# Optimization experiments

Hardware: AMD Instinct MI355X
Metric: run time of the kernel (lower is better)

The kernel has to match this reference:

```python
import jax, jax.numpy as jnp
import numpy as np

M = 0.4
S = 64.0
EPS = 1e-5

def _normalize(x, axis=-1):
    n = jnp.linalg.norm(x, axis=axis, keepdims=True)
    return x / jnp.maximum(n, EPS)

def setup_inputs() -> dict:
    key = jax.random.key(0)
    k1, k2, k3 = jax.random.split(key, 3)
    B, D, C = 512, 512, 100000
    inp = jax.random.normal(k1, (B, D), dtype=jnp.float32)
    weight = jax.random.normal(k2, (C, D), dtype=jnp.float32) * (D ** -0.5)
    label = jax.random.randint(k3, (B,), 0, C, dtype=jnp.int64)
    bias = jnp.full((1,), float(np.log(C * 10)), dtype=jnp.float32)
    return {"input": inp, "label": label, "weight": weight, "bias": bias}

def reference(input, label, weight, bias):
    # cos_theta: [B, C]
    cos_theta = _normalize(input) @ _normalize(weight).T
    cos_m_theta_p = S * (cos_theta - M) - bias
    cos_m_theta_n = S * cos_theta - bias
    # log(1 + exp(x)) with clamp to [-S, S] as in the original
    p_loss = jnp.log1p(jnp.exp(-jnp.clip(cos_m_theta_p, -S, S)))
    n_loss = jnp.log1p(jnp.exp(jnp.clip(cos_m_theta_n, -S, S)))
    one_hot = jax.nn.one_hot(label, cos_theta.shape[1], dtype=jnp.bool_)
    losses = jnp.where(one_hot, p_loss, n_loss)
    return losses.sum(axis=1).mean()
```

## Files before the change

### kernel.cpp

```cpp
#include <hip/hip_runtime.h>
#include <hip/hip_bf16.h>
#include <stdint.h>

#define C_CLS  100000
#define DDIM   512
#define BROWS  512
#define NT     64
#define NSTEP  16
#define EPSN   1e-5f

typedef __attribute__((ext_vector_type(8))) short short8;
typedef __attribute__((ext_vector_type(4))) float f32x4;


__device__ inline unsigned pk2(float a, float b) {
  __hip_bfloat162 h = __float22bfloat162_rn(make_float2(a, b));
  unsigned u; __builtin_memcpy(&u, &h, 4); return u;
}

__global__ void __launch_bounds__(64) k_norm_input(const float* __restrict__ in,
                                                   uint4* __restrict__ xnf,
                                                   float* __restrict__ ws) {
  int b = blockIdx.x;
  int lane = threadIdx.x;
  if (lane == 0) {
    if (b < 256) ws[b * 16] = 0.f;
    else if (b < 320) ws[4096 + (b - 256) * 16] = 0.f;
  }
  const float4* row = (const float4*)(in + b * DDIM);
  float4 v0 = row[lane * 2];
  float4 v1 = row[lane * 2 + 1];
  float ss = v0.x*v0.x + v0.y*v0.y + v0.z*v0.z + v0.w*v0.w
           + v1.x*v1.x + v1.y*v1.y + v1.z*v1.z + v1.w*v1.w;
#pragma unroll
  for (int o = 32; o >= 1; o >>= 1) ss += __shfl_xor(ss, o, 64);
  float sc = 1.f / fmaxf(sqrtf(ss), EPSN);
  uint4 o4;
  o4.x = pk2(v0.x*sc, v0.y*sc);
  o4.y = pk2(v0.z*sc, v0.w*sc);
  o4.z = pk2(v1.x*sc, v1.y*sc);
  o4.w = pk2(v1.z*sc, v1.w*sc);
  int idx = ((lane >> 2) * 32 + (b >> 4)) * 64 + (lane & 3) * 16 + (b & 15);
  xnf[idx] = o4;
}

__global__ void __launch_bounds__(512, 4) k_gemm(const uint4* __restrict__ xnf,
                                                 const float* __restrict__ wt,
                                                 const float* __restrict__ bias,
                                                 float* __restrict__ ws) {
  __shared__ __align__(16) unsigned char sW[NSTEP][4096];
  __shared__ float sNsq[NT];
  __shared__ float sRed[8];

  const int tid  = threadIdx.x;
  const int lane = tid & 63;
  const int wv   = tid >> 6;
  const int cbase = blockIdx.x * NT;

  const int rbyte = (lane * 16) ^ (((lane >> 4) & 3) << 4);
  const uint4* abase = xnf + wv * 256 + lane;

  short8 afA[4], afB[4];
#pragma unroll
  for (int m = 0; m < 4; m++)
    afA[m] = *(const short8*)(abase + m * 64);

  const int cls = tid >> 3;
  const int qb  = tid & 7;
  int wcls = cbase + cls;
  if (wcls >= C_CLS) wcls = C_CLS - 1;
  const float4* wsrc = (const float4*)(wt + (size_t)wcls * DDIM) + qb;
  const int kh_ = (qb >> 1) & 3;
  const int wbyte = (cls >> 4) * 1024 + kh_ * 256
                  + (((cls & 15) * 16) ^ (kh_ << 4)) + (qb & 1) * 8;

  float wsq = 0.f;
  {
    float4 wr0[8], wr1[8];
#pragma unroll
    for (int j = 0; j < 8; ++j) wr0[j] = wsrc[j * 8];
#pragma unroll
    for (int j = 0; j < 8; ++j) wr1[j] = wsrc[(8 + j) * 8];
#pragma unroll
    for (int j = 0; j < 8; ++j) {
      float4 w = wr0[j];
      wsq += w.x*w.x + w.y*w.y + w.z*w.z + w.w*w.w;
      uint2 d; d.x = pk2(w.x, w.y); d.y = pk2(w.z, w.w);
      *(uint2*)(sW[j] + wbyte) = d;
    }
#pragma unroll
    for (int j = 0; j < 8; ++j) {
      float4 w = wr1[j];
      wsq += w.x*w.x + w.y*w.y + w.z*w.z + w.w*w.w;
      uint2 d; d.x = pk2(w.x, w.y); d.y = pk2(w.z, w.w);
      *(uint2*)(sW[8 + j] + wbyte) = d;
    }
  }
#pragma unroll
  for (int o = 1; o < 8; o <<= 1) wsq += __shfl_xor(wsq, o, 64);
  if (qb == 0) sNsq[cls] = wsq;
  __syncthreads();

  f32x4 acc[4][4];
#pragma unroll
  for (int m = 0; m < 4; m++)
#pragma unroll
    for (int n = 0; n < 4; n++) acc[m][n] = (f32x4)(0.f);

  auto loadA = [&](short8* af, int s) {
#pragma unroll
    for (int m = 0; m < 4; m++)
      af[m] = *(const short8*)(abase + s * 2048 + m * 64);
  };
  auto compute = [&](int s, const short8* af) {
    const unsigned char* Wb = sW[s];
#pragma unroll
    for (int n = 0; n < 4; n++) {
      short8 wf = *(const short8*)(Wb + n * 1024 + rbyte);
#pragma unroll
      for (int m = 0; m < 4; m++)
        acc[m][n] = __builtin_amdgcn_mfma_f32_16x16x32_bf16(af[m], wf, acc[m][n], 0, 0, 0);
    }
  };

#pragma unroll 1
  for (int s2 = 0; s2 < NSTEP / 2; ++s2) {
    int s0 = s2 * 2;
    loadA(afB, s0 + 1);
    compute(s0, afA);
    if (s2 < NSTEP / 2 - 1) loadA(afA, s0 + 2);
    compute(s0 + 1, afB);
  }

  const float bv = bias[0];
  float sum = 0.f;
#pragma unroll
  for (int n = 0; n < 4; n++) {
    int cl = n * 16 + (lane & 15);
    float s64 = 64.f / fmaxf(sqrtf(sNsq[cl]), EPSN);
    bool valid = (cbase + cl) < C_CLS;
#pragma unroll
    for (int m = 0; m < 4; m++) {
#pragma unroll
      for (int i = 0; i < 4; i++) {
        float x = fmaf(acc[m][n][i], s64, -bv);
        float z = __expf(x);
        float l = fmaf(-0.5f * z, z, z);
        if (z > 0.03125f) l = __logf(1.f + z);
        sum += valid ? l : 0.f;
      }
    }
  }
#pragma unroll
  for (int o = 32; o >= 1; o >>= 1) sum += __shfl_xor(sum, o, 64);
  if (lane == 0) sRed[wv] = sum;
  __syncthreads();
  if (tid == 0) {
    float t = 0.f;
#pragma unroll
    for (int i = 0; i < 8; i++) t += sRed[i];
    atomicAdd(&ws[(blockIdx.x & 255) * 16], t);
  }
}

__global__ void __launch_bounds__(64) k_label(const float* __restrict__ in,
                                              const float* __restrict__ wt,
                                              const int* __restrict__ label,
                                              const float* __restrict__ bias,
                                              float* __restrict__ ws) {
  int b = blockIdx.x;
  int lane = threadIdx.x;
  int c = label[b];
  const float4* xr = (const float4*)(in + b * DDIM);
  const float4* wr = (const float4*)(wt + (size_t)c * DDIM);
  float dt = 0.f, sx = 0.f, sw = 0.f;
#pragma unroll
  for (int i = 0; i < 2; i++) {
    float4 x = xr[lane * 2 + i];
    float4 w = wr[lane * 2 + i];
    dt += x.x*w.x + x.y*w.y + x.z*w.z + x.w*w.w;
    sx += x.x*x.x + x.y*x.y + x.z*x.z + x.w*x.w;
    sw += w.x*w.x + w.y*w.y + w.z*w.z + w.w*w.w;
  }
#pragma unroll
  for (int o = 32; o >= 1; o >>= 1) {
    dt += __shfl_xor(dt, o, 64);
    sx += __shfl_xor(sx, o, 64);
    sw += __shfl_xor(sw, o, 64);
  }
  if (lane == 0) {
    float bv = bias[0];
    float cosv = dt / (fmaxf(sqrtf(sx), EPSN) * fmaxf(sqrtf(sw), EPSN));
    float cp = 64.f * (cosv - 0.4f) - bv;
    cp = fminf(fmaxf(cp, -64.f), 64.f);
    float pl = log1pf(expf(-cp));
    float cn = 64.f * cosv - bv;
    cn = fminf(fmaxf(cn, -64.f), 64.f);
    float nl = log1pf(expf(cn));
    atomicAdd(&ws[4096 + (b & 63) * 16], pl - nl);
  }
}

__global__ void __launch_bounds__(64) k_final(const float* __restrict__ ws,
                                              float* __restrict__ out) {
  int lane = threadIdx.x;
  float s = ws[lane * 16] + ws[(lane + 64) * 16]
          + ws[(lane + 128) * 16] + ws[(lane + 192) * 16]
          + ws[4096 + lane * 16];
#pragma unroll
  for (int o = 32; o >= 1; o >>= 1) s += __shfl_xor(s, o, 64);
  if (lane == 0) out[0] = s * (1.f / 512.f);
}

extern "C" void kernel_launch(void* const* d_in, const int* in_sizes, int n_in,
                              void* d_out, int out_size, void* d_ws, size_t ws_size,
                              hipStream_t stream) {
  const float* input  = (const float*)d_in[0];
  const int*   label  = (const int*)d_in[1];
  const float* weight = (const float*)d_in[2];
  const float* bias   = (const float*)d_in[3];
  float* out = (float*)d_out;
  float* ws  = (float*)d_ws;
  uint4* xnf = (uint4*)((char*)d_ws + 32768);

  k_norm_input<<<BROWS, 64, 0, stream>>>(input, xnf, ws);
  k_gemm<<<(C_CLS + NT - 1) / NT, 512, 0, stream>>>(xnf, weight, bias, ws);
  k_label<<<BROWS, 64, 0, stream>>>(input, weight, label, bias, ws);
  k_final<<<1, 64, 0, stream>>>(ws, out);
}
```

Before: 96.89 us.

## Make GEMM persistent with double-buffered weight staging and larger per-wave tiles

```diff
diff --git a/kernel.cpp b/kernel.cpp
--- a/kernel.cpp
+++ b/kernel.cpp
@@ -6,8 +6,8 @@
 #define DDIM   512
 #define BROWS  512
 #define NT     64
-#define NSTEP  16
 #define EPSN   1e-5f
+#define GRID_G 512
 
 typedef __attribute__((ext_vector_type(8))) short short8;
 typedef __attribute__((ext_vector_type(4))) float f32x4;
@@ -44,123 +44,156 @@
   xnf[idx] = o4;
 }
 
-__global__ void __launch_bounds__(512, 4) k_gemm(const uint4* __restrict__ xnf,
-                                                 const float* __restrict__ wt,
-                                                 const float* __restrict__ bias,
-                                                 float* __restrict__ ws) {
-  __shared__ __align__(16) unsigned char sW[NSTEP][4096];
-  __shared__ float sNsq[NT];
-  __shared__ float sRed[8];
+__global__ void __launch_bounds__(256, 2)
+k_gemm(const uint4* __restrict__ xnf, const float* __restrict__ wt,
+       const float* __restrict__ bias, float* __restrict__ ws) {
+  __shared__ __align__(16) unsigned char sH[2][32768];
+  __shared__ float sNsq[2][NT];
+  __shared__ float sRed[4];
 
   const int tid  = threadIdx.x;
   const int lane = tid & 63;
   const int wv   = tid >> 6;
-  const int cbase = blockIdx.x * NT;
-
+  const int b    = blockIdx.x;
+  const int ntile = (b < 27) ? 4 : 3;
+  const int P = ntile * 2;
+
+  const int c_loc = tid >> 2;
+  const int sub   = tid & 3;
   const int rbyte = (lane * 16) ^ (((lane >> 4) & 3) << 4);
-  const uint4* abase = xnf + wv * 256 + lane;
-
-  short8 afA[4], afB[4];
-#pragma unroll
-  for (int m = 0; m < 4; m++)
-    afA[m] = *(const short8*)(abase + m * 64);
-
-  const int cls = tid >> 3;
-  const int qb  = tid & 7;
-  int wcls = cbase + cls;
-  if (wcls >= C_CLS) wcls = C_CLS - 1;
-  const float4* wsrc = (const float4*)(wt + (size_t)wcls * DDIM) + qb;
-  const int kh_ = (qb >> 1) & 3;
-  const int wbyte = (cls >> 4) * 1024 + kh_ * 256
-                  + (((cls & 15) * 16) ^ (kh_ << 4)) + (qb & 1) * 8;
-
-  float wsq = 0.f;
-  {
-    float4 wr0[8], wr1[8];
-#pragma unroll
-    for (int j = 0; j < 8; ++j) wr0[j] = wsrc[j * 8];
-#pragma unroll
-    for (int j = 0; j < 8; ++j) wr1[j] = wsrc[(8 + j) * 8];
+
+  float wsq = 0.f, lsum = 0.f;
+  const float bv = bias[0];
+
+  auto stage_write = [&](unsigned char* dst, const float4* wr, int batch) {
 #pragma unroll
     for (int j = 0; j < 8; ++j) {
-      float4 w = wr0[j];
+      int q = sub + 4 * (batch * 8 + j);
+      int kh = (q >> 1) & 3;
+      int cell = (c_loc >> 4) * 64 + kh * 16 + (c_loc & 15);
+      int byte = (q >> 3) * 4096 + ((cell * 16) ^ (kh << 4)) + (q & 1) * 8;
+      float4 w = wr[j];
       wsq += w.x*w.x + w.y*w.y + w.z*w.z + w.w*w.w;
       uint2 d; d.x = pk2(w.x, w.y); d.y = pk2(w.z, w.w);
-      *(uint2*)(sW[j] + wbyte) = d;
-    }
-#pragma unroll
-    for (int j = 0; j < 8; ++j) {
-      float4 w = wr1[j];
-      wsq += w.x*w.x + w.y*w.y + w.z*w.z + w.w*w.w;
-      uint2 d; d.x = pk2(w.x, w.y); d.y = pk2(w.z, w.w);
-      *(uint2*)(sW[8 + j] + wbyte) = d;
-    }
-  }
-#pragma unroll
-  for (int o = 1; o < 8; o <<= 1) wsq += __shfl_xor(wsq, o, 64);
-  if (qb == 0) sNsq[cls] = wsq;
+      *(uint2*)(dst + byte) = d;
+    }
+  };
+
+  {
+    int cls = b * NT + c_loc;
+    if (cls >= C_CLS) cls = C_CLS - 1;
+    const float4* src = (const float4*)(wt + (size_t)cls * DDIM);
+    float4 wr[8];
+#pragma unroll
+    for (int j = 0; j < 8; ++j) wr[j] = src[sub + 4 * j];
+    stage_write(sH[0], wr, 0);
+#pragma unroll
+    for (int j = 0; j < 8; ++j) wr[j] = src[sub + 4 * (8 + j)];
+    stage_write(sH[0], wr, 1);
+  }
+
+  f32x4 acc[8][4];
+#pragma unroll
+  for (int m = 0; m < 8; ++m)
+#pragma unroll
+    for (int n = 0; n < 4; ++n) acc[m][n] = (f32x4)(0.f);
+
   __syncthreads();
 
-  f32x4 acc[4][4];
-#pragma unroll
-  for (int m = 0; m < 4; m++)
-#pragma unroll
-    for (int n = 0; n < 4; n++) acc[m][n] = (f32x4)(0.f);
-
-  auto loadA = [&](short8* af, int s) {
-#pragma unroll
-    for (int m = 0; m < 4; m++)
-      af[m] = *(const short8*)(abase + s * 2048 + m * 64);
-  };
-  auto compute = [&](int s, const short8* af) {
-    const unsigned char* Wb = sW[s];
-#pragma unroll
-    for (int n = 0; n < 4; n++) {
-      short8 wf = *(const short8*)(Wb + n * 1024 + rbyte);
-#pragma unroll
-      for (int m = 0; m < 4; m++)
-        acc[m][n] = __builtin_amdgcn_mfma_f32_16x16x32_bf16(af[m], wf, acc[m][n], 0, 0, 0);
-    }
-  };
-
 #pragma unroll 1
-  for (int s2 = 0; s2 < NSTEP / 2; ++s2) {
-    int s0 = s2 * 2;
-    loadA(afB, s0 + 1);
-    compute(s0, afA);
-    if (s2 < NSTEP / 2 - 1) loadA(afA, s0 + 2);
-    compute(s0 + 1, afB);
-  }
-
-  const float bv = bias[0];
-  float sum = 0.f;
-#pragma unroll
-  for (int n = 0; n < 4; n++) {
-    int cl = n * 16 + (lane & 15);
-    float s64 = 64.f / fmaxf(sqrtf(sNsq[cl]), EPSN);
-    bool valid = (cbase + cl) < C_CLS;
-#pragma unroll
-    for (int m = 0; m < 4; m++) {
-#pragma unroll
-      for (int i = 0; i < 4; i++) {
-        float x = fmaf(acc[m][n][i], s64, -bv);
-        float z = __expf(x);
-        float l = fmaf(-0.5f * z, z, z);
-        if (z > 0.03125f) l = __logf(1.f + z);
-        sum += valid ? l : 0.f;
-      }
-    }
-  }
-#pragma unroll
-  for (int o = 32; o >= 1; o >>= 1) sum += __shfl_xor(sum, o, 64);
-  if (lane == 0) sRed[wv] = sum;
+  for (int p = 0; p < P; ++p) {
+    const int cur = p & 1;
+    const bool more = (p + 1 < P);
+    const float4* src1 = nullptr;
+    if (more) {
+      int t1 = (p + 1) >> 1, h1 = (p + 1) & 1;
+      int cls = (b + t1 * GRID_G) * NT + c_loc;
+      if (cls >= C_CLS) cls = C_CLS - 1;
+      src1 = (const float4*)(wt + (size_t)cls * DDIM + h1 * 256);
+    }
+    float4 wr[8];
+    if (more) {
+#pragma unroll
+      for (int j = 0; j < 8; ++j) wr[j] = src1[sub + 4 * j];
+    }
+#pragma unroll
+    for (int sl = 0; sl < 4; ++sl) {
+      int s = cur * 8 + sl;
+      const uint4* ab = xnf + ((s * 32 + wv * 8) * 64 + lane);
+      short8 af[8];
+#pragma unroll
+      for (int m = 0; m < 8; ++m) af[m] = *(const short8*)(ab + m * 64);
+      const unsigned char* Wb = sH[cur] + sl * 4096;
+#pragma unroll
+      for (int n = 0; n < 4; ++n) {
+        short8 wf = *(const short8*)(Wb + n * 1024 + rbyte);
+#pragma unroll
+        for (int m = 0; m < 8; ++m)
+          acc[m][n] = __builtin_amdgcn_mfma_f32_16x16x32_bf16(af[m], wf, acc[m][n], 0, 0, 0);
+      }
+    }
+    if (more) {
+      stage_write(sH[cur ^ 1], wr, 0);
+#pragma unroll
+      for (int j = 0; j < 8; ++j) wr[j] = src1[sub + 4 * (8 + j)];
+    }
+#pragma unroll
+    for (int sl = 4; sl < 8; ++sl) {
+      int s = cur * 8 + sl;
+      const uint4* ab = xnf + ((s * 32 + wv * 8) * 64 + lane);
+      short8 af[8];
+#pragma unroll
+      for (int m = 0; m < 8; ++m) af[m] = *(const short8*)(ab + m * 64);
+      const unsigned char* Wb = sH[cur] + sl * 4096;
+#pragma unroll
+      for (int n = 0; n < 4; ++n) {
+        short8 wf = *(const short8*)(Wb + n * 1024 + rbyte);
+#pragma unroll
+        for (int m = 0; m < 8; ++m)
+          acc[m][n] = __builtin_amdgcn_mfma_f32_16x16x32_bf16(af[m], wf, acc[m][n], 0, 0, 0);
+      }
+    }
+    if (cur == 1) {
+      int t = p >> 1;
+      int cb = (b + t * GRID_G) * NT;
+      const float* nsq = sNsq[t & 1];
+#pragma unroll
+      for (int n = 0; n < 4; ++n) {
+        int cl = n * 16 + (lane & 15);
+        float s64 = 64.f / fmaxf(sqrtf(nsq[cl]), EPSN);
+        bool valid = (cb + cl) < C_CLS;
+#pragma unroll
+        for (int m = 0; m < 8; ++m) {
+#pragma unroll
+          for (int i = 0; i < 4; ++i) {
+            float x = fmaf(acc[m][n][i], s64, -bv);
+            float z = __expf(x);
+            float l = fmaf(-0.5f * z, z, z);
+            if (z > 0.03125f) l = __logf(1.f + z);
+            lsum += valid ? l : 0.f;
+          }
+          acc[m][n] = (f32x4)(0.f);
+        }
+      }
+    }
+    if (more) {
+      stage_write(sH[cur ^ 1], wr, 1);
+      if (((p + 1) & 1) == 1) {
+        float t2 = wsq + __shfl_xor(wsq, 1, 64);
+        t2 += __shfl_xor(t2, 2, 64);
+        if (sub == 0) sNsq[((p + 1) >> 1) & 1][c_loc] = t2;
+        wsq = 0.f;
+      }
+    }
+    __syncthreads();
+  }
+
+#pragma unroll
+  for (int o = 32; o >= 1; o >>= 1) lsum += __shfl_xor(lsum, o, 64);
+  if (lane == 0) sRed[wv] = lsum;
   __syncthreads();
-  if (tid == 0) {
-    float t = 0.f;
-#pragma unroll
-    for (int i = 0; i < 8; i++) t += sRed[i];
-    atomicAdd(&ws[(blockIdx.x & 255) * 16], t);
-  }
+  if (tid == 0)
+    atomicAdd(&ws[(b & 255) * 16], sRed[0] + sRed[1] + sRed[2] + sRed[3]);
 }
 
 __global__ void __launch_bounds__(64) k_label(const float* __restrict__ in,
@@ -224,7 +257,7 @@
   uint4* xnf = (uint4*)((char*)d_ws + 32768);
 
   k_norm_input<<<BROWS, 64, 0, stream>>>(input, xnf, ws);
-  k_gemm<<<(C_CLS + NT - 1) / NT, 512, 0, stream>>>(xnf, weight, bias, ws);
+  k_gemm<<<GRID_G, 256, 0, stream>>>(xnf, weight, bias, ws);
   k_label<<<BROWS, 64, 0, stream>>>(input, weight, label, bias, ws);
   k_final<<<1, 64, 0, stream>>>(ws, out);
 }
```

Measured after the change: 119.9 us. +23.8%, slower.

## Stream weight fragments from global into registers, dropping LDS staging

Applied to the files above, without the earlier changes.

```diff
diff --git a/kernel.cpp b/kernel.cpp
--- a/kernel.cpp
+++ b/kernel.cpp
@@ -44,101 +44,98 @@
   xnf[idx] = o4;
 }
 
-__global__ void __launch_bounds__(512, 4) k_gemm(const uint4* __restrict__ xnf,
-                                                 const float* __restrict__ wt,
-                                                 const float* __restrict__ bias,
-                                                 float* __restrict__ ws) {
-  __shared__ __align__(16) unsigned char sW[NSTEP][4096];
-  __shared__ float sNsq[NT];
-  __shared__ float sRed[8];
-
+__global__ void __launch_bounds__(512, 2)
+k_gemm(const uint4* __restrict__ xnf, const float* __restrict__ wt,
+       const float* __restrict__ bias, float* __restrict__ ws) {
   const int tid  = threadIdx.x;
   const int lane = tid & 63;
   const int wv   = tid >> 6;
   const int cbase = blockIdx.x * NT;
 
-  const int rbyte = (lane * 16) ^ (((lane >> 4) & 3) << 4);
-  const uint4* abase = xnf + wv * 256 + lane;
-
-  short8 afA[4], afB[4];
+  const int wrow_ = lane & 15;
+  const int koff  = (lane >> 4) * 8;
+
+  auto rowp = [&](int n) {
+    int c = cbase + n * 16 + wrow_;
+    if (c >= C_CLS) c = C_CLS - 1;
+    return wt + (size_t)c * DDIM + koff;
+  };
+  const float* wp0 = rowp(0);
+  const float* wp1 = rowp(1);
+  const float* wp2 = rowp(2);
+  const float* wp3 = rowp(3);
+
+  const uint4* abase = xnf + (wv * 4) * 64 + lane;
+
+  float4 wA[8], wB[8];
+  short8 aA[4], aB[4];
+  short8 wf[4];
+  float wsq[4] = {0.f, 0.f, 0.f, 0.f};
+  f32x4 acc[4][4];
 #pragma unroll
   for (int m = 0; m < 4; m++)
-    afA[m] = *(const short8*)(abase + m * 64);
-
-  const int cls = tid >> 3;
-  const int qb  = tid & 7;
-  int wcls = cbase + cls;
-  if (wcls >= C_CLS) wcls = C_CLS - 1;
-  const float4* wsrc = (const float4*)(wt + (size_t)wcls * DDIM) + qb;
-  const int kh_ = (qb >> 1) & 3;
-  const int wbyte = (cls >> 4) * 1024 + kh_ * 256
-                  + (((cls & 15) * 16) ^ (kh_ << 4)) + (qb & 1) * 8;
-
-  float wsq = 0.f;
-  {
-    float4 wr0[8], wr1[8];
-#pragma unroll
-    for (int j = 0; j < 8; ++j) wr0[j] = wsrc[j * 8];
-#pragma unroll
-    for (int j = 0; j < 8; ++j) wr1[j] = wsrc[(8 + j) * 8];
-#pragma unroll
-    for (int j = 0; j < 8; ++j) {
-      float4 w = wr0[j];
-      wsq += w.x*w.x + w.y*w.y + w.z*w.z + w.w*w.w;
-      uint2 d; d.x = pk2(w.x, w.y); d.y = pk2(w.z, w.w);
-      *(uint2*)(sW[j] + wbyte) = d;
+#pragma unroll
+    for (int n = 0; n < 4; n++) acc[m][n] = (f32x4)(0.f);
+
+  auto loadW = [&](float4 (&w)[8], int s) {
+    const int o = s * 32;
+    w[0] = *(const float4*)(wp0 + o); w[1] = *(const float4*)(wp0 + o + 4);
+    w[2] = *(const float4*)(wp1 + o); w[3] = *(const float4*)(wp1 + o + 4);
+    w[4] = *(const float4*)(wp2 + o); w[5] = *(const float4*)(wp2 + o + 4);
+    w[6] = *(const float4*)(wp3 + o); w[7] = *(const float4*)(wp3 + o + 4);
+  };
+  auto loadA = [&](short8 (&af)[4], int s) {
+    const uint4* p = abase + s * 2048;
+#pragma unroll
+    for (int m = 0; m < 4; m++)
+      af[m] = *(const short8*)(p + m * 64);
+  };
+  auto cvtW = [&](const float4 (&w)[8]) {
+#pragma unroll
+    for (int n = 0; n < 4; n++) {
+      float4 a = w[n * 2], b = w[n * 2 + 1];
+      wsq[n] += a.x*a.x + a.y*a.y + a.z*a.z + a.w*a.w
+              + b.x*b.x + b.y*b.y + b.z*b.z + b.w*b.w;
+      uint4 u;
+      u.x = pk2(a.x, a.y); u.y = pk2(a.z, a.w);
+      u.z = pk2(b.x, b.y); u.w = pk2(b.z, b.w);
+      __builtin_memcpy(&wf[n], &u, 16);
     }
-#pragma unroll
-    for (int j = 0; j < 8; ++j) {
-      float4 w = wr1[j];
-      wsq += w.x*w.x + w.y*w.y + w.z*w.z + w.w*w.w;
-      uint2 d; d.x = pk2(w.x, w.y); d.y = pk2(w.z, w.w);
-      *(uint2*)(sW[8 + j] + wbyte) = d;
-    }
-  }
-#pragma unroll
-  for (int o = 1; o < 8; o <<= 1) wsq += __shfl_xor(wsq, o, 64);
-  if (qb == 0) sNsq[cls] = wsq;
-  __syncthreads();
-
-  f32x4 acc[4][4];
-#pragma unroll
-  for (int m = 0; m < 4; m++)
-#pragma unroll
-    for (int n = 0; n < 4; n++) acc[m][n] = (f32x4)(0.f);
-
-  auto loadA = [&](short8* af, int s) {
-#pragma unroll
-    for (int m = 0; m < 4; m++)
-      af[m] = *(const short8*)(abase + s * 2048 + m * 64);
-  };
-  auto compute = [&](int s, const short8* af) {
-    const unsigned char* Wb = sW[s];
-#pragma unroll
-    for (int n = 0; n < 4; n++) {
-      short8 wf = *(const short8*)(Wb + n * 1024 + rbyte);
+  };
+  auto domfma = [&](const short8 (&af)[4]) {
+#pragma unroll
+    for (int n = 0; n < 4; n++)
 #pragma unroll
       for (int m = 0; m < 4; m++)
-        acc[m][n] = __builtin_amdgcn_mfma_f32_16x16x32_bf16(af[m], wf, acc[m][n], 0, 0, 0);
-    }
-  };
+        acc[m][n] = __builtin_amdgcn_mfma_f32_16x16x32_bf16(af[m], wf[n], acc[m][n], 0, 0, 0);
+  };
+
+  loadW(wA, 0);
+  loadW(wB, 1);
+  loadA(aA, 0);
 
 #pragma unroll 1
-  for (int s2 = 0; s2 < NSTEP / 2; ++s2) {
-    int s0 = s2 * 2;
-    loadA(afB, s0 + 1);
-    compute(s0, afA);
-    if (s2 < NSTEP / 2 - 1) loadA(afA, s0 + 2);
-    compute(s0 + 1, afB);
+  for (int s2 = 0; s2 < 8; ++s2) {
+    const int s0 = s2 * 2;
+    loadA(aB, s0 + 1);
+    cvtW(wA);
+    if (s2 < 7) loadW(wA, s0 + 2);
+    domfma(aA);
+    if (s2 < 7) loadA(aA, s0 + 2);
+    cvtW(wB);
+    if (s2 < 7) loadW(wB, s0 + 3);
+    domfma(aB);
   }
 
   const float bv = bias[0];
-  float sum = 0.f;
+  float lsum = 0.f;
 #pragma unroll
   for (int n = 0; n < 4; n++) {
-    int cl = n * 16 + (lane & 15);
-    float s64 = 64.f / fmaxf(sqrtf(sNsq[cl]), EPSN);
-    bool valid = (cbase + cl) < C_CLS;
+    float t = wsq[n];
+    t += __shfl_xor(t, 16, 64);
+    t += __shfl_xor(t, 32, 64);
+    float s64 = 64.f / fmaxf(sqrtf(t), EPSN);
+    bool valid = (cbase + n * 16 + wrow_) < C_CLS;
 #pragma unroll
     for (int m = 0; m < 4; m++) {
 #pragma unroll
@@ -147,20 +144,13 @@
         float z = __expf(x);
         float l = fmaf(-0.5f * z, z, z);
         if (z > 0.03125f) l = __logf(1.f + z);
-        sum += valid ? l : 0.f;
+        lsum += valid ? l : 0.f;
       }
     }
   }
 #pragma unroll
-  for (int o = 32; o >= 1; o >>= 1) sum += __shfl_xor(sum, o, 64);
-  if (lane == 0) sRed[wv] = sum;
-  __syncthreads();
-  if (tid == 0) {
-    float t = 0.f;
-#pragma unroll
-    for (int i = 0; i < 8; i++) t += sRed[i];
-    atomicAdd(&ws[(blockIdx.x & 255) * 16], t);
-  }
+  for (int o = 32; o >= 1; o >>= 1) lsum += __shfl_xor(lsum, o, 64);
+  if (lane == 0) atomicAdd(&ws[(blockIdx.x & 255) * 16], lsum);
 }
 
 __global__ void __launch_bounds__(64) k_label(const float* __restrict__ in,
```

New measurement: 281.6 us. 2.91x slower.

## Stage weight rows via direct global-to-LDS loads and overlap second half with MFMA

Applied to the files above, without the earlier changes.

```diff
diff --git a/kernel.cpp b/kernel.cpp
--- a/kernel.cpp
+++ b/kernel.cpp
@@ -44,11 +44,11 @@
   xnf[idx] = o4;
 }
 
-__global__ void __launch_bounds__(512, 4) k_gemm(const uint4* __restrict__ xnf,
-                                                 const float* __restrict__ wt,
-                                                 const float* __restrict__ bias,
-                                                 float* __restrict__ ws) {
-  __shared__ __align__(16) unsigned char sW[NSTEP][4096];
+__global__ void __launch_bounds__(512, 2)
+k_gemm(const uint4* __restrict__ xnf, const float* __restrict__ wt,
+       const float* __restrict__ bias, float* __restrict__ ws) {
+  __shared__ __align__(16) unsigned char sF[NT * 1024];
+  __shared__ __align__(16) unsigned char sW[NSTEP * 4096];
   __shared__ float sNsq[NT];
   __shared__ float sRed[8];
 
@@ -57,83 +57,79 @@
   const int wv   = tid >> 6;
   const int cbase = blockIdx.x * NT;
 
-  const int rbyte = (lane * 16) ^ (((lane >> 4) & 3) << 4);
+  auto dmaHalf = [&](int h) {
+#pragma unroll
+    for (int i = 0; i < 8; ++i) {
+      int c = i * 8 + wv;
+      int cc = cbase + c;
+      if (cc >= C_CLS) cc = C_CLS - 1;
+      const float* src = wt + (size_t)cc * DDIM + h * 256 + lane * 4;
+      __builtin_amdgcn_global_load_lds(
+          (const __attribute__((address_space(1))) unsigned int*)src,
+          (__attribute__((address_space(3))) unsigned int*)(sF + c * 1024),
+          16, 0, 0);
+    }
+  };
+
+  auto cvtHalf = [&](int h) {
+#pragma unroll
+    for (int p = 0; p < 8; ++p) {
+      int c = p * 8 + wv;
+      float4 v = *(const float4*)(sF + c * 1024 + lane * 16);
+      float sq = v.x*v.x + v.y*v.y + v.z*v.z + v.w*v.w;
+#pragma unroll
+      for (int o = 32; o >= 1; o >>= 1) sq += __shfl_xor(sq, o, 64);
+      int s  = h * 8 + (lane >> 3);
+      int kh = (lane & 7) >> 1;
+      int cell = ((c >> 4) * 64 + kh * 16 + (c & 15)) * 16;
+      int byte = (cell ^ (((kh ^ s) & 3) << 4)) + (lane & 1) * 8;
+      uint2 d; d.x = pk2(v.x, v.y); d.y = pk2(v.z, v.w);
+      *(uint2*)(sW + s * 4096 + byte) = d;
+      if (lane == 0) { if (h) sNsq[c] += sq; else sNsq[c] = sq; }
+    }
+  };
+
+  f32x4 acc[4][4];
+#pragma unroll
+  for (int m = 0; m < 4; m++)
+#pragma unroll
+    for (int n = 0; n < 4; n++) acc[m][n] = (f32x4)(0.f);
+
   const uint4* abase = xnf + wv * 256 + lane;
 
-  short8 afA[4], afB[4];
-#pragma unroll
-  for (int m = 0; m < 4; m++)
-    afA[m] = *(const short8*)(abase + m * 64);
-
-  const int cls = tid >> 3;
-  const int qb  = tid & 7;
-  int wcls = cbase + cls;
-  if (wcls >= C_CLS) wcls = C_CLS - 1;
-  const float4* wsrc = (const float4*)(wt + (size_t)wcls * DDIM) + qb;
-  const int kh_ = (qb >> 1) & 3;
-  const int wbyte = (cls >> 4) * 1024 + kh_ * 256
-                  + (((cls & 15) * 16) ^ (kh_ << 4)) + (qb & 1) * 8;
-
-  float wsq = 0.f;
-  {
-    float4 wr0[8], wr1[8];
-#pragma unroll
-    for (int j = 0; j < 8; ++j) wr0[j] = wsrc[j * 8];
-#pragma unroll
-    for (int j = 0; j < 8; ++j) wr1[j] = wsrc[(8 + j) * 8];
-#pragma unroll
-    for (int j = 0; j < 8; ++j) {
-      float4 w = wr0[j];
-      wsq += w.x*w.x + w.y*w.y + w.z*w.z + w.w*w.w;
-      uint2 d; d.x = pk2(w.x, w.y); d.y = pk2(w.z, w.w);
-      *(uint2*)(sW[j] + wbyte) = d;
-    }
-#pragma unroll
-    for (int j = 0; j < 8; ++j) {
-      float4 w = wr1[j];
-      wsq += w.x*w.x + w.y*w.y + w.z*w.z + w.w*w.w;
-      uint2 d; d.x = pk2(w.x, w.y); d.y = pk2(w.z, w.w);
-      *(uint2*)(sW[8 + j] + wbyte) = d;
-    }
-  }
-#pragma unroll
-  for (int o = 1; o < 8; o <<= 1) wsq += __shfl_xor(wsq, o, 64);
-  if (qb == 0) sNsq[cls] = wsq;
-  __syncthreads();
-
-  f32x4 acc[4][4];
-#pragma unroll
-  for (int m = 0; m < 4; m++)
-#pragma unroll
-    for (int n = 0; n < 4; n++) acc[m][n] = (f32x4)(0.f);
-
-  auto loadA = [&](short8* af, int s) {
-#pragma unroll
-    for (int m = 0; m < 4; m++)
-      af[m] = *(const short8*)(abase + s * 2048 + m * 64);
+  auto computeHalf = [&](int h) {
+#pragma unroll 2
+    for (int sl = 0; sl < 8; ++sl) {
+      int s = h * 8 + sl;
+      short8 af[4];
+#pragma unroll
+      for (int m = 0; m < 4; m++)
+        af[m] = *(const short8*)(abase + s * 2048 + m * 64);
+      const unsigned char* Wb = sW + s * 4096;
+      const int rbyte = (lane * 16) ^ ((((lane >> 4) ^ s) & 3) << 4);
+#pragma unroll
+      for (int n = 0; n < 4; n++) {
+        short8 wf = *(const short8*)(Wb + n * 1024 + rbyte);
+#pragma unroll
+        for (int m = 0; m < 4; m++)
+          acc[m][n] = __builtin_amdgcn_mfma_f32_16x16x32_bf16(af[m], wf, acc[m][n], 0, 0, 0);
+      }
+    }
   };
-  auto compute = [&](int s, const short8* af) {
-    const unsigned char* Wb = sW[s];
-#pragma unroll
-    for (int n = 0; n < 4; n++) {
-      short8 wf = *(const short8*)(Wb + n * 1024 + rbyte);
-#pragma unroll
-      for (int m = 0; m < 4; m++)
-        acc[m][n] = __builtin_amdgcn_mfma_f32_16x16x32_bf16(af[m], wf, acc[m][n], 0, 0, 0);
-    }
-  };
-
-#pragma unroll 1
-  for (int s2 = 0; s2 < NSTEP / 2; ++s2) {
-    int s0 = s2 * 2;
-    loadA(afB, s0 + 1);
-    compute(s0, afA);
-    if (s2 < NSTEP / 2 - 1) loadA(afA, s0 + 2);
-    compute(s0 + 1, afB);
-  }
+
+  dmaHalf(0);
+  __syncthreads();
+  cvtHalf(0);
+  __syncthreads();
+  dmaHalf(1);
+  computeHalf(0);
+  __syncthreads();
+  cvtHalf(1);
+  __syncthreads();
+  computeHalf(1);
 
   const float bv = bias[0];
-  float sum = 0.f;
+  float lsum = 0.f;
 #pragma unroll
   for (int n = 0; n < 4; n++) {
     int cl = n * 16 + (lane & 15);
@@ -147,13 +143,13 @@
         float z = __expf(x);
         float l = fmaf(-0.5f * z, z, z);
         if (z > 0.03125f) l = __logf(1.f + z);
-        sum += valid ? l : 0.f;
+        lsum += valid ? l : 0.f;
       }
     }
   }
 #pragma unroll
-  for (int o = 32; o >= 1; o >>= 1) sum += __shfl_xor(sum, o, 64);
-  if (lane == 0) sRed[wv] = sum;
+  for (int o = 32; o >= 1; o >>= 1) lsum += __shfl_xor(lsum, o, 64);
+  if (lane == 0) sRed[wv] = lsum;
   __syncthreads();
   if (tid == 0) {
     float t = 0.f;
```

After: 161.0 us. 1.66x slower.
